# Performance work log

Measured on AMD Instinct MI355X. Metric: run time of the kernel, lower is better.

The kernel has to match this reference:

```python
import jax, jax.numpy as jnp
import numpy as np

DOF = 7
B = 8192
DT = 0.1
ACTION_RANGE = 50.0
MAX_VEL = 20.0


def _skew(w):
    x, y, z = w[..., 0], w[..., 1], w[..., 2]
    O = jnp.zeros_like(x)
    return jnp.stack([jnp.stack([O, -z, y], -1),
                      jnp.stack([z, O, -x], -1),
                      jnp.stack([-y, x, O], -1)], -2)


def _exp_se3(xi):
    # xi: (..., 6) twist [w; v] (already scaled by joint angle) -> (..., 4, 4)
    w, v = xi[..., :3], xi[..., 3:]
    th = jnp.sqrt(jnp.sum(w * w, -1))
    small = th < 1e-4
    ths = jnp.where(small, 1.0, th)  # safe denominator
    th2 = th * th
    a = jnp.where(small, 1.0 - th2 / 6.0, jnp.sin(th) / ths)
    b = jnp.where(small, 0.5 - th2 / 24.0, (1.0 - jnp.cos(th)) / (ths * ths))
    c = jnp.where(small, 1.0 / 6.0 - th2 / 120.0, (th - jnp.sin(th)) / (ths * ths * ths))
    K = _skew(w)
    K2 = K @ K
    I3 = jnp.eye(3, dtype=xi.dtype)
    R = I3 + a[..., None, None] * K + b[..., None, None] * K2
    Vm = I3 + b[..., None, None] * K + c[..., None, None] * K2
    p = jnp.einsum('...ij,...j->...i', Vm, v)
    top = jnp.concatenate([R, p[..., None]], -1)
    bot = jnp.broadcast_to(jnp.array([0.0, 0.0, 0.0, 1.0], xi.dtype), top.shape[:-2] + (1, 4))
    return jnp.concatenate([top, bot], -2)


def _inv_T(T):
    R = T[..., :3, :3]
    p = T[..., :3, 3]
    Rt = jnp.swapaxes(R, -1, -2)
    pn = -jnp.einsum('...ij,...j->...i', Rt, p)
    top = jnp.concatenate([Rt, pn[..., None]], -1)
    bot = jnp.broadcast_to(jnp.array([0.0, 0.0, 0.0, 1.0], T.dtype), top.shape[:-2] + (1, 4))
    return jnp.concatenate([top, bot], -2)


def _adjoint(T):
    # SE(3) adjoint for [w; v] twists: [[R, 0], [ [p]x R, R ]]
    R = T[..., :3, :3]
    p = T[..., :3, 3]
    pR = _skew(p) @ R
    Z = jnp.zeros_like(R)
    return jnp.concatenate([jnp.concatenate([R, Z], -1),
                            jnp.concatenate([pR, R], -1)], -2)


def _ad(V):
    # se(3) little adjoint: [[ [w]x, 0 ], [ [v]x, [w]x ]]
    Kw = _skew(V[..., :3])
    Kv = _skew(V[..., 3:])
    Z = jnp.zeros_like(Kw)
    return jnp.concatenate([jnp.concatenate([Kw, Z], -1),
                            jnp.concatenate([Kv, Kw], -1)], -2)


def _inverse_dynamics(q, dq, ddq, g, Ftip, M, G, A):
    # Recursive Newton-Euler (Modern Robotics, link-frame screws A).
    Bq, n = q.shape
    V = jnp.zeros((Bq, 6), q.dtype)
    Vd = jnp.broadcast_to(jnp.concatenate([jnp.zeros(3, q.dtype), -g]), (Bq, 6))
    AdTs, Vs, Vds = [], [], []
    for i in range(n):
        T = _exp_se3(-A[i] * q[:, i, None]) @ _inv_T(M[i])  # T_{i,i-1}, (B,4,4)
        AdT = _adjoint(T)
        V = jnp.einsum('bij,bj->bi', AdT, V) + A[i] * dq[:, i, None]
        Vd = (jnp.einsum('bij,bj->bi', AdT, Vd)
              + jnp.einsum('bij,j->bi', _ad(V), A[i]) * dq[:, i, None]
              + A[i] * ddq[:, i, None])
        AdTs.append(AdT)
        Vs.append(V)
        Vds.append(Vd)
    F = jnp.broadcast_to(Ftip.astype(q.dtype), (Bq, 6))
    AdT_end = _adjoint(_inv_T(M[n]))  # T_{n+1,n}, (6,6)
    taus = [None] * n
    for i in range(n - 1, -1, -1):
        if i == n - 1:
            F = jnp.einsum('ji,bj->bi', AdT_end, F)
        else:
            F = jnp.einsum('bji,bj->bi', AdTs[i + 1], F)
        F = (F + jnp.einsum('ij,bj->bi', G[i], Vds[i])
             - jnp.einsum('bji,jk,bk->bi', _ad(Vs[i]), G[i], Vs[i]))
        taus[i] = jnp.einsum('bi,i->b', F, A[i])
    return jnp.stack(taus, -1)  # (B, n)


def _forward_dynamics(q, dq, tau, g, Ftip, M, G, A):
    n = q.shape[1]
    zer = jnp.zeros_like(q)
    # bias forces: Coriolis + gravity + end-effector wrench
    h = _inverse_dynamics(q, dq, zer, g, Ftip, M, G, A)
    g0 = jnp.zeros(3, q.dtype)
    f0 = jnp.zeros(6, q.dtype)
    # mass matrix columns via unit accelerations (vmapped over columns)
    cols = jax.vmap(lambda e: _inverse_dynamics(
        q, zer, jnp.broadcast_to(e, q.shape), g0, f0, M, G, A))(jnp.eye(n, dtype=q.dtype))
    Mmat = jnp.transpose(cols, (1, 2, 0))  # (B, n, n)
    return jnp.linalg.solve(Mmat, (tau - h)[..., None])[..., 0]


def _fk_in_space(q, M, A):
    Bq, n = q.shape
    T = jnp.broadcast_to(jnp.eye(4, dtype=q.dtype), (Bq, 4, 4))
    outs = []
    for i in range(n):
        T = (T @ M[i]) @ _exp_se3(A[i] * q[:, i, None])
        outs.append(T)
    outs.append(T @ M[n])
    return jnp.stack(outs, 1)  # (B, n+1, 4, 4)


def setup_inputs():
    key = jax.random.key(0)
    ks = jax.random.split(key, 4)
    state = jax.random.normal(ks[0], (B, 2 * DOF), jnp.float32)
    torque = jax.random.normal(ks[1], (B, DOF), jnp.float32)
    M = jnp.tile(jnp.eye(4, dtype=jnp.float32)[None], (DOF + 1, 1, 1))
    A = jax.random.uniform(ks[2], (DOF, 6), jnp.float32)
    L = jax.random.normal(ks[3], (DOF, 6, 6), jnp.float32)
    gravity = jnp.array([0.0, -9.8, 0.0], jnp.float32)
    ftip = jnp.zeros(6, jnp.float32)
    return {"state": state, "torque": torque, "M": M, "A": A, "L": L,
            "gravity": gravity, "ftip": ftip}


def reference(state, torque, M, A, L, gravity, ftip):
    n = DOF
    G = L @ jnp.swapaxes(L, -1, -2)  # spatial inertias, PSD
    s0 = jnp.concatenate([state, torque * ACTION_RANGE], -1)  # (B, 3n)

    def derivs(s):
        q = s[..., :n]
        dq = s[..., n:2 * n]
        qf = s[..., 2 * n:]
        qacc = _forward_dynamics(q, dq, qf, gravity, ftip, M, G, A)
        return jnp.concatenate([dq, qacc, jnp.zeros_like(qf)], -1)

    k1 = derivs(s0)
    k2 = derivs(s0 + 0.5 * DT * k1)
    k3 = derivs(s0 + 0.5 * DT * k2)
    k4 = derivs(s0 + DT * k3)
    s1 = s0 + (DT / 6.0) * (k1 + 2.0 * k2 + 2.0 * k3 + k4)
    q = jnp.mod(s1[..., :n] + jnp.pi, 2.0 * jnp.pi) - jnp.pi
    dq = jnp.clip(s1[..., n:2 * n], -MAX_VEL, MAX_VEL)
    ee = _fk_in_space(q, M, A)
    return jnp.concatenate([q, dq], -1), ee[:, -1, :2, 3]
```

## Files before the change

kernel.cpp:

```cpp
#include <hip/hip_runtime.h>
#include <hip/hip_bf16.h>

#define DTC 0.1f
#define ACTION_RANGE 50.0f
#define MAX_VEL 20.0f
#define PI_F 3.14159265358979323846f
#define TWO_PI_F 6.28318530717958647692f
#define INV_TWO_PI_F 0.15915494309189533577f

__device__ __forceinline__ float bf2f(__hip_bfloat16 x){ return __bfloat162float(x); }
__device__ __forceinline__ float frcp(float x){ return __builtin_amdgcn_rcpf(x); }

__device__ __forceinline__ float ldv(const void* p, int i, bool isb){
  return isb ? __bfloat162float(((const __hip_bfloat16*)p)[i]) : ((const float*)p)[i];
}
__device__ __forceinline__ void stv(void* p, int i, float v, bool isb){
  if (isb) ((__hip_bfloat16*)p)[i] = __float2bfloat16(v);
  else     ((float*)p)[i] = v;
}

__device__ __forceinline__ void exp_se3_Rp(const float* Aj, float s, float* R, float* P){
  float wx=Aj[0]*s, wy=Aj[1]*s, wz=Aj[2]*s;
  float vx=Aj[3]*s, vy=Aj[4]*s, vz=Aj[5]*s;
  float th2 = wx*wx+wy*wy+wz*wz;
  float th = sqrtf(th2);
  float th4 = th2*th2;
  float aS = 1.f - th2*(1.f/6.f)  + th4*(1.f/120.f);
  float bS = 0.5f - th2*(1.f/24.f) + th4*(1.f/720.f);
  float cS = (1.f/6.f) - th2*(1.f/120.f) + th4*(1.f/5040.f);
  float sn = __sinf(th), cs = __cosf(th);
  float inv = frcp(th), inv2 = inv*inv;
  float aL = sn*inv;
  float bL = (1.f-cs)*inv2;
  float cL = (th-sn)*inv2*inv;
  bool sm = th < 0.25f;
  float a = sm?aS:aL, b = sm?bS:bL, c = sm?cS:cL;
  R[0]=1.f+b*(wx*wx-th2); R[1]=b*wx*wy-a*wz;      R[2]=b*wx*wz+a*wy;
  R[3]=b*wx*wy+a*wz;      R[4]=1.f+b*(wy*wy-th2); R[5]=b*wy*wz-a*wx;
  R[6]=b*wx*wz-a*wy;      R[7]=b*wy*wz+a*wx;      R[8]=1.f+b*(wz*wz-th2);
  float V0=1.f+c*(wx*wx-th2), V1=c*wx*wy-b*wz,      V2=c*wx*wz+b*wy;
  float V3=c*wx*wy+b*wz,      V4=1.f+c*(wy*wy-th2), V5=c*wy*wz-b*wx;
  float V6=c*wx*wz-b*wy,      V7=c*wy*wz+b*wx,      V8=1.f+c*(wz*wz-th2);
  P[0]=V0*vx+V1*vy+V2*vz;
  P[1]=V3*vx+V4*vy+V5*vz;
  P[2]=V6*vx+V7*vy+V8*vz;
}

__device__ __forceinline__ void mul33(const float* X, const float* Y, float* Z){
  #pragma unroll
  for (int r=0;r<3;r++){
    float x0=X[r*3+0], x1=X[r*3+1], x2=X[r*3+2];
    Z[r*3+0]=x0*Y[0]+x1*Y[3]+x2*Y[6];
    Z[r*3+1]=x0*Y[1]+x1*Y[4]+x2*Y[7];
    Z[r*3+2]=x0*Y[2]+x1*Y[5]+x2*Y[8];
  }
}

__device__ __forceinline__ void ad_apply(const float* R, const float* p, const float* Vin, float* Vout){
  float i0=Vin[0],i1=Vin[1],i2=Vin[2],i3=Vin[3],i4=Vin[4],i5=Vin[5];
  float w0 = R[0]*i0+R[1]*i1+R[2]*i2;
  float w1 = R[3]*i0+R[4]*i1+R[5]*i2;
  float w2 = R[6]*i0+R[7]*i1+R[8]*i2;
  float r0 = R[0]*i3+R[1]*i4+R[2]*i5;
  float r1 = R[3]*i3+R[4]*i4+R[5]*i5;
  float r2 = R[6]*i3+R[7]*i4+R[8]*i5;
  float p0=p[0],p1=p[1],p2=p[2];
  Vout[0]=w0; Vout[1]=w1; Vout[2]=w2;
  Vout[3]=p1*w2-p2*w1+r0;
  Vout[4]=p2*w0-p0*w2+r1;
  Vout[5]=p0*w1-p1*w0+r2;
}

__device__ __forceinline__ void adT_apply(const float* R, const float* p, const float* Fin, float* Fout){
  float m0=Fin[0],m1=Fin[1],m2=Fin[2],f0=Fin[3],f1=Fin[4],f2=Fin[5];
  float p0=p[0],p1=p[1],p2=p[2];
  float cx = m0 - (p1*f2 - p2*f1);
  float cy = m1 - (p2*f0 - p0*f2);
  float cz = m2 - (p0*f1 - p1*f0);
  float o0 = R[0]*cx + R[3]*cy + R[6]*cz;
  float o1 = R[1]*cx + R[4]*cy + R[7]*cz;
  float o2 = R[2]*cx + R[5]*cy + R[8]*cz;
  float o3 = R[0]*f0 + R[3]*f1 + R[6]*f2;
  float o4 = R[1]*f0 + R[4]*f1 + R[7]*f2;
  float o5 = R[2]*f0 + R[5]*f1 + R[8]*f2;
  Fout[0]=o0;Fout[1]=o1;Fout[2]=o2;Fout[3]=o3;Fout[4]=o4;Fout[5]=o5;
}

__device__ __forceinline__ void gmatvec2_sym(const float* Gu, const float* v, const float* d,
                                             float* gv, float* gvd){
  float g0=Gu[0],g1=Gu[1],g2=Gu[2],g3=Gu[3],g4=Gu[4],g5=Gu[5];
  float g6=Gu[6],g7=Gu[7],g8=Gu[8],g9=Gu[9],g10=Gu[10];
  float g11=Gu[11],g12=Gu[12],g13=Gu[13],g14=Gu[14];
  float g15=Gu[15],g16=Gu[16],g17=Gu[17],g18=Gu[18],g19=Gu[19],g20=Gu[20];
  gv[0]=g0*v[0]+g1 *v[1]+g2 *v[2]+g3 *v[3]+g4 *v[4]+g5 *v[5];
  gv[1]=g1*v[0]+g6 *v[1]+g7 *v[2]+g8 *v[3]+g9 *v[4]+g10*v[5];
  gv[2]=g2*v[0]+g7 *v[1]+g11*v[2]+g12*v[3]+g13*v[4]+g14*v[5];
  gv[3]=g3*v[0]+g8 *v[1]+g12*v[2]+g15*v[3]+g16*v[4]+g17*v[5];
  gv[4]=g4*v[0]+g9 *v[1]+g13*v[2]+g16*v[3]+g18*v[4]+g19*v[5];
  gv[5]=g5*v[0]+g10*v[1]+g14*v[2]+g17*v[3]+g19*v[4]+g20*v[5];
  gvd[0]=g0*d[0]+g1 *d[1]+g2 *d[2]+g3 *d[3]+g4 *d[4]+g5 *d[5];
  gvd[1]=g1*d[0]+g6 *d[1]+g7 *d[2]+g8 *d[3]+g9 *d[4]+g10*d[5];
  gvd[2]=g2*d[0]+g7 *d[1]+g11*d[2]+g12*d[3]+g13*d[4]+g14*d[5];
  gvd[3]=g3*d[0]+g8 *d[1]+g12*d[2]+g15*d[3]+g16*d[4]+g17*d[5];
  gvd[4]=g4*d[0]+g9 *d[1]+g13*d[2]+g16*d[3]+g18*d[4]+g19*d[5];
  gvd[5]=g5*d[0]+g10*d[1]+g14*d[2]+g17*d[3]+g19*d[4]+g20*d[5];
}

#define W_STRIDE 100

__global__ __launch_bounds__(64) void arm_rk4_kernel(
    const void* __restrict__ g_state,
    const void* __restrict__ g_torque,
    const void* __restrict__ g_M,
    const void* __restrict__ g_A,
    const void* __restrict__ g_L,
    const void* __restrict__ g_grav,
    const void* __restrict__ g_ftip,
    void* __restrict__ g_out,
    int B)
{
  __shared__ float sA[42];
  __shared__ __align__(16) float sGu[168];
  __shared__ float sMinvR[72];
  __shared__ float sMinvp[24];
  __shared__ float sMR[72];
  __shared__ float sMp[24];
  __shared__ float sgrav[3];
  __shared__ float sftip[6];
  __shared__ __align__(16) float sW[8*W_STRIDE];

  const bool isb = fabsf(bf2f(((const __hip_bfloat16*)g_grav)[1]) + 9.8f) < 0.5f;

  const int t = threadIdx.x;
  for (int x=t; x<42; x+=64) sA[x] = ldv(g_A, x, isb);
  for (int x=t; x<168; x+=64){
    int i = x/24; int u = x - i*24;
    if (u < 21){
      int rr = 0, u2 = u;
      while (u2 >= 6-rr){ u2 -= 6-rr; rr++; }
      int cc = rr + u2;
      float s = 0.f;
      #pragma unroll
      for (int k=0;k<6;k++) s += ldv(g_L, i*36+rr*6+k, isb) * ldv(g_L, i*36+cc*6+k, isb);
      sGu[x] = s;
    } else {
      sGu[x] = 0.f;
    }
  }
  if (t < 8){
    float R[9], p[3];
    #pragma unroll
    for (int rr=0;rr<3;rr++){
      #pragma unroll
      for (int cc=0;cc<3;cc++) R[rr*3+cc] = ldv(g_M, t*16 + rr*4 + cc, isb);
      p[rr] = ldv(g_M, t*16 + rr*4 + 3, isb);
    }
    #pragma unroll
    for (int rr=0;rr<3;rr++){
      #pragma unroll
      for (int cc=0;cc<3;cc++){ sMR[t*9+rr*3+cc] = R[rr*3+cc]; sMinvR[t*9+rr*3+cc] = R[cc*3+rr]; }
      sMp[t*3+rr] = p[rr];
      sMinvp[t*3+rr] = -(R[0*3+rr]*p[0] + R[1*3+rr]*p[1] + R[2*3+rr]*p[2]);
    }
  }
  if (t == 0){ for (int k=0;k<3;k++) sgrav[k] = ldv(g_grav, k, isb); }
  if (t == 1){ for (int k=0;k<6;k++) sftip[k] = ldv(g_ftip, k, isb); }
  __syncthreads();

  const int e = t >> 3;
  const int r = t & 7;
  int b = blockIdx.x * 8 + e;
  if (b >= B) b = B - 1;
  const bool is7 = (r == 7);
  float* W = &sW[e*W_STRIDE];

  float q0[7], dq0[7], qf[7];
  #pragma unroll
  for (int i=0;i<7;i++){
    q0[i]  = ldv(g_state, b*14+i, isb);
    dq0[i] = ldv(g_state, b*14+7+i, isb);
    qf[i]  = ldv(g_torque, b*7+i, isb) * ACTION_RANGE;
  }
  float kq[7], kdd[7], accq[7], accdq[7];
  #pragma unroll
  for (int i=0;i<7;i++){ kq[i]=0.f; kdd[i]=0.f; accq[i]=0.f; accdq[i]=0.f; }

  float Fend[6];
  {
    float tf[6]; adT_apply(&sMinvR[63], &sMinvp[21], sftip, tf);
    #pragma unroll
    for (int k=0;k<6;k++) Fend[k] = is7 ? tf[k] : 0.f;
  }

  #pragma unroll 1
  for (int st=0; st<4; ++st){
    const float cin = (st==0) ? 0.f : ((st==3) ? DTC : 0.5f*DTC);
    const float wgt = (st==0||st==3) ? (DTC/6.f) : (DTC/3.f);
    float qs[7], dqs[7];
    #pragma unroll
    for (int i=0;i<7;i++){ qs[i]=q0[i]+cin*kq[i]; dqs[i]=dq0[i]+cin*kdd[i]; }

    float qsr = 0.f;
    #pragma unroll
    for (int c=0;c<7;c++) qsr = (r==c) ? qs[c] : qsr;

    if (r < 7){
      float Re[9], Pe[3], Rt[9];
      exp_se3_Rp(&sA[r*6], -qsr, Re, Pe);
      mul33(Re, &sMinvR[r*9], Rt);
      float Tw[12];
      #pragma unroll
      for (int k=0;k<9;k++) Tw[k] = Rt[k];
      #pragma unroll
      for (int rr=0;rr<3;rr++)
        Tw[9+rr] = Re[rr*3+0]*sMinvp[r*3+0] + Re[rr*3+1]*sMinvp[r*3+1]
                 + Re[rr*3+2]*sMinvp[r*3+2] + Pe[rr];
      #pragma unroll
      for (int k=0;k<12;k++) W[r*12+k] = Tw[k];
    }
    __syncthreads();

    float sacc[7][6];
    float V[6] = {0,0,0,0,0,0};
    float Vd[6];
    Vd[0]=0.f; Vd[1]=0.f; Vd[2]=0.f;
    Vd[3] = is7 ? -sgrav[0] : 0.f;
    Vd[4] = is7 ? -sgrav[1] : 0.f;
    Vd[5] = is7 ? -sgrav[2] : 0.f;
    #pragma unroll
    for (int i=0;i<7;i++){
      float Tl[12];
      #pragma unroll
      for (int k=0;k<12;k++) Tl[k] = W[i*12+k];
      const float* R = Tl;
      const float* p = Tl+9;
      float dqi  = is7 ? dqs[i] : 0.f;
      float ddqi = is7 ? 0.f : ((r==i) ? 1.f : 0.f);
      ad_apply(R,p,V,V);
      #pragma unroll
      for (int k=0;k<6;k++) V[k] += sA[i*6+k]*dqi;
      ad_apply(R,p,Vd,Vd);
      {
        float w0=V[0],w1=V[1],w2=V[2],v0=V[3],v1=V[4],v2=V[5];
        float a0=sA[i*6+0],a1=sA[i*6+1],a2=sA[i*6+2],a3=sA[i*6+3],a4=sA[i*6+4],a5=sA[i*6+5];
        Vd[0] += (w1*a2-w2*a1)*dqi + a0*ddqi;
        Vd[1] += (w2*a0-w0*a2)*dqi + a1*ddqi;
        Vd[2] += (w0*a1-w1*a0)*dqi + a2*ddqi;
        Vd[3] += ((v1*a2-v2*a1)+(w1*a5-w2*a4))*dqi + a3*ddqi;
        Vd[4] += ((v2*a0-v0*a2)+(w2*a3-w0*a5))*dqi + a4*ddqi;
        Vd[5] += ((v0*a1-v1*a0)+(w0*a4-w1*a3))*dqi + a5*ddqi;
      }
      float gv[6], gvd[6];
      gmatvec2_sym(&sGu[i*24], V, Vd, gv, gvd);
      {
        float w0=V[0],w1=V[1],w2=V[2],v0=V[3],v1=V[4],v2=V[5];
        sacc[i][0] = gvd[0] + (w1*gv[2]-w2*gv[1]) + (v1*gv[5]-v2*gv[4]);
        sacc[i][1] = gvd[1] + (w2*gv[0]-w0*gv[2]) + (v2*gv[3]-v0*gv[5]);
        sacc[i][2] = gvd[2] + (w0*gv[1]-w1*gv[0]) + (v0*gv[4]-v1*gv[3]);
        sacc[i][3] = gvd[3] + (w1*gv[5]-w2*gv[4]);
        sacc[i][4] = gvd[4] + (w2*gv[3]-w0*gv[5]);
        sacc[i][5] = gvd[5] + (w0*gv[4]-w1*gv[3]);
      }
    }

    float m[7];
    {
      float F[6];
      #pragma unroll
      for (int k=0;k<6;k++) F[k] = Fend[k];
      #pragma unroll
      for (int i=6;i>=0;i--){
        if (i<6){
          float Tl[12];
          #pragma unroll
          for (int k=0;k<12;k++) Tl[k] = W[(i+1)*12+k];
          adT_apply(Tl, Tl+9, F, F);
        }
        #pragma unroll
        for (int k=0;k<6;k++) F[k] += sacc[i][k];
        m[i] = F[0]*sA[i*6+0]+F[1]*sA[i*6+1]+F[2]*sA[i*6+2]
             + F[3]*sA[i*6+3]+F[4]*sA[i*6+4]+F[5]*sA[i*6+5];
      }
    }

    float U[7][7];
    #pragma unroll
    for (int i=0;i<7;i++){
      #pragma unroll
      for (int j=i;j<7;j++) U[i][j] = __shfl(m[j], i, 8);
    }
    float rv[7];
    #pragma unroll
    for (int i=0;i<7;i++) rv[i] = qf[i] - __shfl(m[i], 7, 8);
    #pragma unroll
    for (int k=0;k<7;k++){
      float dinv = frcp(U[k][k]);
      #pragma unroll
      for (int i=k+1;i<7;i++){
        float f = U[k][i]*dinv;
        #pragma unroll
        for (int j=i;j<7;j++) U[i][j] -= f*U[k][j];
        rv[i] -= f*rv[k];
      }
    }
    float x[7];
    #pragma unroll
    for (int i=6;i>=0;i--){
      float s = rv[i];
      #pragma unroll
      for (int j=i+1;j<7;j++) s -= U[i][j]*x[j];
      x[i] = s*frcp(U[i][i]);
    }

    #pragma unroll
    for (int i=0;i<7;i++){
      kq[i]  = dqs[i];
      kdd[i] = x[i];
      accq[i]  += wgt*dqs[i];
      accdq[i] += wgt*x[i];
    }
    __syncthreads();
  }

  float q1r=0.f, dq1r=0.f;
  #pragma unroll
  for (int c=0;c<7;c++){
    float xx = q0[c] + accq[c] + PI_F;
    float mm = xx - floorf(xx * INV_TWO_PI_F) * TWO_PI_F;
    float qv = mm - PI_F;
    float dv = dq0[c] + accdq[c];
    dv = fminf(fmaxf(dv, -MAX_VEL), MAX_VEL);
    q1r  = (r==c) ? qv : q1r;
    dq1r = (r==c) ? dv : dq1r;
  }

  {
    float XR[9], Xp[3];
    if (r < 7){
      float Re[9], Pe[3];
      exp_se3_Rp(&sA[r*6], q1r, Re, Pe);
      mul33(&sMR[r*9], Re, XR);
      #pragma unroll
      for (int rr=0;rr<3;rr++)
        Xp[rr] = sMR[r*9+rr*3+0]*Pe[0]+sMR[r*9+rr*3+1]*Pe[1]+sMR[r*9+rr*3+2]*Pe[2] + sMp[r*3+rr];
    } else {
      #pragma unroll
      for (int k=0;k<9;k++) XR[k] = sMR[63+k];
      #pragma unroll
      for (int k=0;k<3;k++) Xp[k] = sMp[21+k];
    }
    #pragma unroll
    for (int k=0;k<9;k++) W[r*12+k]   = XR[k];
    #pragma unroll
    for (int k=0;k<3;k++) W[r*12+9+k] = Xp[k];
  }
  __syncthreads();

  #pragma unroll
  for (int w=4; w>=1; w>>=1){
    float Ra[9], pa[3], Rb[9], pb[3];
    if (r < w){
      #pragma unroll
      for (int k=0;k<9;k++){ Ra[k]=W[(2*r)*12+k]; Rb[k]=W[(2*r+1)*12+k]; }
      #pragma unroll
      for (int k=0;k<3;k++){ pa[k]=W[(2*r)*12+9+k]; pb[k]=W[(2*r+1)*12+9+k]; }
    }
    __syncthreads();
    if (r < w){
      float Rc[9];
      mul33(Ra, Rb, Rc);
      #pragma unroll
      for (int k=0;k<9;k++) W[r*12+k] = Rc[k];
      #pragma unroll
      for (int rr=0;rr<3;rr++)
        W[r*12+9+rr] = Ra[rr*3+0]*pb[0]+Ra[rr*3+1]*pb[1]+Ra[rr*3+2]*pb[2] + pa[rr];
    }
    __syncthreads();
  }

  if (r < 7){
    stv(g_out, b*14+r,   q1r,  isb);
    stv(g_out, b*14+7+r, dq1r, isb);
  } else {
    stv(g_out, B*14 + b*2 + 0, W[9],  isb);
    stv(g_out, B*14 + b*2 + 1, W[10], isb);
  }
}

extern "C" void kernel_launch(void* const* d_in, const int* in_sizes, int n_in,
                              void* d_out, int out_size, void* d_ws, size_t ws_size,
                              hipStream_t stream) {
  const int B = in_sizes[0] / 14;
  const int blocks = (B + 7) / 8;
  arm_rk4_kernel<<<blocks, 64, 0, stream>>>(d_in[0], d_in[1], d_in[2], d_in[3],
                                            d_in[4], d_in[5], d_in[6], d_out, B);
}
```

Measured before the change: 100.7 us.

## Spill RNEA per-link forces and mass-matrix columns to LDS to cut register pressure

The per-link spatial force accumulators (sacc) and mass-matrix column values are moved from registers into shared memory. The forward and backward RNEA loops are no longer unrolled, and the shuffle-based gather of mass-matrix entries becomes LDS reads. Joint velocities are staged in LDS so the non-unrolled loop can index them, and the screw-axis table is padded to 8 floats per joint for aligned loads. The aim is to cut VGPR usage, but it adds LDS traffic, extra barriers and loop overhead.

```diff
diff --git a/kernel.cpp b/kernel.cpp
--- a/kernel.cpp
+++ b/kernel.cpp
@@ -119,7 +119,7 @@
     void* __restrict__ g_out,
     int B)
 {
-  __shared__ float sA[42];
+  __shared__ __align__(16) float sA8[56];
   __shared__ __align__(16) float sGu[168];
   __shared__ float sMinvR[72];
   __shared__ float sMinvp[24];
@@ -128,11 +128,17 @@
   __shared__ float sgrav[3];
   __shared__ float sftip[6];
   __shared__ __align__(16) float sW[8*W_STRIDE];
+  __shared__ float sacc_lds[7*6*64];
+  __shared__ float m_lds[7*64];
+  __shared__ float dqs_lds[7*8];
 
   const bool isb = fabsf(bf2f(((const __hip_bfloat16*)g_grav)[1]) + 9.8f) < 0.5f;
 
   const int t = threadIdx.x;
-  for (int x=t; x<42; x+=64) sA[x] = ldv(g_A, x, isb);
+  for (int x=t; x<56; x+=64){
+    int i = x >> 3, k = x & 7;
+    sA8[x] = (k < 6) ? ldv(g_A, i*6+k, isb) : 0.f;
+  }
   for (int x=t; x<168; x+=64){
     int i = x/24; int u = x - i*24;
     if (u < 21){
@@ -143,9 +149,7 @@
       #pragma unroll
       for (int k=0;k<6;k++) s += ldv(g_L, i*36+rr*6+k, isb) * ldv(g_L, i*36+cc*6+k, isb);
       sGu[x] = s;
-    } else {
-      sGu[x] = 0.f;
-    }
+    } else sGu[x] = 0.f;
   }
   if (t < 8){
     float R[9], p[3];
@@ -204,9 +208,14 @@
     #pragma unroll
     for (int c=0;c<7;c++) qsr = (r==c) ? qs[c] : qsr;
 
+    if (is7){
+      #pragma unroll
+      for (int i=0;i<7;i++) dqs_lds[i*8+e] = dqs[i];
+    }
+
     if (r < 7){
       float Re[9], Pe[3], Rt[9];
-      exp_se3_Rp(&sA[r*6], -qsr, Re, Pe);
+      exp_se3_Rp(&sA8[r*8], -qsr, Re, Pe);
       mul33(Re, &sMinvR[r*9], Rt);
       float Tw[12];
       #pragma unroll
@@ -220,55 +229,60 @@
     }
     __syncthreads();
 
-    float sacc[7][6];
     float V[6] = {0,0,0,0,0,0};
     float Vd[6];
     Vd[0]=0.f; Vd[1]=0.f; Vd[2]=0.f;
     Vd[3] = is7 ? -sgrav[0] : 0.f;
     Vd[4] = is7 ? -sgrav[1] : 0.f;
     Vd[5] = is7 ? -sgrav[2] : 0.f;
-    #pragma unroll
+    #pragma unroll 1
     for (int i=0;i<7;i++){
       float Tl[12];
       #pragma unroll
       for (int k=0;k<12;k++) Tl[k] = W[i*12+k];
-      const float* R = Tl;
-      const float* p = Tl+9;
-      float dqi  = is7 ? dqs[i] : 0.f;
-      float ddqi = is7 ? 0.f : ((r==i) ? 1.f : 0.f);
-      ad_apply(R,p,V,V);
-      #pragma unroll
-      for (int k=0;k<6;k++) V[k] += sA[i*6+k]*dqi;
-      ad_apply(R,p,Vd,Vd);
+      float Al[6];
+      #pragma unroll
+      for (int k=0;k<6;k++) Al[k] = sA8[i*8+k];
+      float dqi  = is7 ? dqs_lds[i*8+e] : 0.f;
+      float ddqi = (!is7 && r==i) ? 1.f : 0.f;
+      ad_apply(Tl, Tl+9, V, V);
+      #pragma unroll
+      for (int k=0;k<6;k++) V[k] += Al[k]*dqi;
+      ad_apply(Tl, Tl+9, Vd, Vd);
       {
         float w0=V[0],w1=V[1],w2=V[2],v0=V[3],v1=V[4],v2=V[5];
-        float a0=sA[i*6+0],a1=sA[i*6+1],a2=sA[i*6+2],a3=sA[i*6+3],a4=sA[i*6+4],a5=sA[i*6+5];
-        Vd[0] += (w1*a2-w2*a1)*dqi + a0*ddqi;
-        Vd[1] += (w2*a0-w0*a2)*dqi + a1*ddqi;
-        Vd[2] += (w0*a1-w1*a0)*dqi + a2*ddqi;
-        Vd[3] += ((v1*a2-v2*a1)+(w1*a5-w2*a4))*dqi + a3*ddqi;
-        Vd[4] += ((v2*a0-v0*a2)+(w2*a3-w0*a5))*dqi + a4*ddqi;
-        Vd[5] += ((v0*a1-v1*a0)+(w0*a4-w1*a3))*dqi + a5*ddqi;
+        Vd[0] += (w1*Al[2]-w2*Al[1])*dqi + Al[0]*ddqi;
+        Vd[1] += (w2*Al[0]-w0*Al[2])*dqi + Al[1]*ddqi;
+        Vd[2] += (w0*Al[1]-w1*Al[0])*dqi + Al[2]*ddqi;
+        Vd[3] += ((v1*Al[2]-v2*Al[1])+(w1*Al[5]-w2*Al[4]))*dqi + Al[3]*ddqi;
+        Vd[4] += ((v2*Al[0]-v0*Al[2])+(w2*Al[3]-w0*Al[5]))*dqi + Al[4]*ddqi;
+        Vd[5] += ((v0*Al[1]-v1*Al[0])+(w0*Al[4]-w1*Al[3]))*dqi + Al[5]*ddqi;
       }
       float gv[6], gvd[6];
       gmatvec2_sym(&sGu[i*24], V, Vd, gv, gvd);
       {
         float w0=V[0],w1=V[1],w2=V[2],v0=V[3],v1=V[4],v2=V[5];
-        sacc[i][0] = gvd[0] + (w1*gv[2]-w2*gv[1]) + (v1*gv[5]-v2*gv[4]);
-        sacc[i][1] = gvd[1] + (w2*gv[0]-w0*gv[2]) + (v2*gv[3]-v0*gv[5]);
-        sacc[i][2] = gvd[2] + (w0*gv[1]-w1*gv[0]) + (v0*gv[4]-v1*gv[3]);
-        sacc[i][3] = gvd[3] + (w1*gv[5]-w2*gv[4]);
-        sacc[i][4] = gvd[4] + (w2*gv[3]-w0*gv[5]);
-        sacc[i][5] = gvd[5] + (w0*gv[4]-w1*gv[3]);
+        float s0 = gvd[0] + (w1*gv[2]-w2*gv[1]) + (v1*gv[5]-v2*gv[4]);
+        float s1 = gvd[1] + (w2*gv[0]-w0*gv[2]) + (v2*gv[3]-v0*gv[5]);
+        float s2 = gvd[2] + (w0*gv[1]-w1*gv[0]) + (v0*gv[4]-v1*gv[3]);
+        float s3 = gvd[3] + (w1*gv[5]-w2*gv[4]);
+        float s4 = gvd[4] + (w2*gv[3]-w0*gv[5]);
+        float s5 = gvd[5] + (w0*gv[4]-w1*gv[3]);
+        sacc_lds[(i*6+0)*64+t] = s0;
+        sacc_lds[(i*6+1)*64+t] = s1;
+        sacc_lds[(i*6+2)*64+t] = s2;
+        sacc_lds[(i*6+3)*64+t] = s3;
+        sacc_lds[(i*6+4)*64+t] = s4;
+        sacc_lds[(i*6+5)*64+t] = s5;
       }
     }
-
-    float m[7];
+    __syncthreads();
+
     {
       float F[6];
       #pragma unroll
       for (int k=0;k<6;k++) F[k] = Fend[k];
-      #pragma unroll
+      #pragma unroll 1
       for (int i=6;i>=0;i--){
         if (i<6){
           float Tl[12];
@@ -277,21 +291,25 @@
           adT_apply(Tl, Tl+9, F, F);
         }
         #pragma unroll
-        for (int k=0;k<6;k++) F[k] += sacc[i][k];
-        m[i] = F[0]*sA[i*6+0]+F[1]*sA[i*6+1]+F[2]*sA[i*6+2]
-             + F[3]*sA[i*6+3]+F[4]*sA[i*6+4]+F[5]*sA[i*6+5];
+        for (int k=0;k<6;k++) F[k] += sacc_lds[(i*6+k)*64+t];
+        float Al[6];
+        #pragma unroll
+        for (int k=0;k<6;k++) Al[k] = sA8[i*8+k];
+        m_lds[i*64+t] = F[0]*Al[0]+F[1]*Al[1]+F[2]*Al[2]
+                      + F[3]*Al[3]+F[4]*Al[4]+F[5]*Al[5];
       }
     }
+    __syncthreads();
 
     float U[7][7];
     #pragma unroll
     for (int i=0;i<7;i++){
       #pragma unroll
-      for (int j=i;j<7;j++) U[i][j] = __shfl(m[j], i, 8);
+      for (int j=i;j<7;j++) U[i][j] = m_lds[j*64 + e*8 + i];
     }
     float rv[7];
     #pragma unroll
-    for (int i=0;i<7;i++) rv[i] = qf[i] - __shfl(m[i], 7, 8);
+    for (int i=0;i<7;i++) rv[i] = qf[i] - m_lds[i*64 + e*8 + 7];
     #pragma unroll
     for (int k=0;k<7;k++){
       float dinv = frcp(U[k][k]);
@@ -338,7 +356,7 @@
     float XR[9], Xp[3];
     if (r < 7){
       float Re[9], Pe[3];
-      exp_se3_Rp(&sA[r*6], q1r, Re, Pe);
+      exp_se3_Rp(&sA8[r*8], q1r, Re, Pe);
       mul33(&sMR[r*9], Re, XR);
       #pragma unroll
       for (int rr=0;rr<3;rr++)
```

Result: faster. 96.47 us (-4.2%).
